# Performance work log

Hardware: AMD Instinct MI355X
Metric: run time of the kernel (lower is better)

Reference implementation:

```python
import jax, jax.numpy as jnp
import numpy as np

M_DIM = 1024
N_HEADS = 16
H_DIM = M_DIM // N_HEADS
FFN_H = 2 * M_DIM
B, S = 2, 2048
EPS = 1e-5
NEG = -1e9


def layernorm(x, g, b):
    mu = jnp.mean(x, axis=-1, keepdims=True)
    var = jnp.mean((x - mu) ** 2, axis=-1, keepdims=True)
    return (x - mu) * jax.lax.rsqrt(var + EPS) * g + b


def setup_inputs() -> dict:
    key = jax.random.key(0)
    ks = jax.random.split(key, 16)
    sc = 0.02
    return {
        "x": jax.random.normal(ks[0], (B, S, M_DIM), jnp.float32),
        "attention_mask": jnp.ones((B, S), jnp.int32),
        # per-head QKV projections stacked over heads: [H, M, D]
        "Wq": jax.random.normal(ks[1], (N_HEADS, M_DIM, H_DIM), jnp.float32) * sc,
        "bq": jnp.zeros((N_HEADS, H_DIM), jnp.float32),
        "Wk": jax.random.normal(ks[2], (N_HEADS, M_DIM, H_DIM), jnp.float32) * sc,
        "bk": jnp.zeros((N_HEADS, H_DIM), jnp.float32),
        "Wv": jax.random.normal(ks[3], (N_HEADS, M_DIM, H_DIM), jnp.float32) * sc,
        "bv": jnp.zeros((N_HEADS, H_DIM), jnp.float32),
        "Wo": jax.random.normal(ks[4], (M_DIM, M_DIM), jnp.float32) * sc,
        "bo": jnp.zeros((M_DIM,), jnp.float32),
        "g1": jnp.ones((M_DIM,), jnp.float32),
        "b1": jnp.zeros((M_DIM,), jnp.float32),
        "W1": jax.random.normal(ks[5], (M_DIM, FFN_H), jnp.float32) * sc,
        "bias1": jnp.zeros((FFN_H,), jnp.float32),
        "W2": jax.random.normal(ks[6], (FFN_H, M_DIM), jnp.float32) * sc,
        "bias2": jnp.zeros((M_DIM,), jnp.float32),
        "g2": jnp.ones((M_DIM,), jnp.float32),
        "b2": jnp.zeros((M_DIM,), jnp.float32),
    }


def reference(x, attention_mask, Wq, bq, Wk, bk, Wv, bv, Wo, bo, g1, b1, W1, bias1, W2, bias2, g2, b2):
    # All heads at once (the torch code loops over heads; same math).
    q = jnp.einsum("bsm,hmd->bhsd", x, Wq) + bq[None, :, None, :]
    k = jnp.einsum("bsm,hmd->bhsd", x, Wk) + bk[None, :, None, :]
    v = jnp.einsum("bsm,hmd->bhsd", x, Wv) + bv[None, :, None, :]
    scores = jnp.einsum("bhqd,bhkd->bhqk", q, k) / jnp.sqrt(jnp.float32(H_DIM))
    mask = attention_mask[:, None, None, :].astype(bool)  # [B,1,1,S] over keys
    scores = jnp.where(mask, scores, NEG)
    attn = jax.nn.softmax(scores, axis=-1)
    ctx = jnp.einsum("bhqk,bhkd->bhqd", attn, v)
    ctx = ctx.transpose(0, 2, 1, 3).reshape(x.shape[0], x.shape[1], M_DIM)  # concat heads
    out = ctx @ Wo + bo
    out = layernorm(out + x, g1, b1)
    fout = jax.nn.relu(out @ W1 + bias1) @ W2 + bias2
    out = layernorm(out + fout, g2, b2)
    return out
```

## Files before the change

kernel.cpp:

```cpp
#include <hip/hip_runtime.h>

#define MDIM 1024
#define FFH  2048
#define SEQ  2048
#define NEGV -1e9f
#define AST  72
#define QSCL 0.18033688f

#if __has_builtin(__builtin_amdgcn_exp2f)
  #define EXP2(x) __builtin_amdgcn_exp2f(x)
#else
  #define EXP2(x) exp2f(x)
#endif

typedef __attribute__((ext_vector_type(8))) __bf16 bf16x8;
typedef __attribute__((ext_vector_type(4))) float floatx4;
typedef __attribute__((address_space(3))) unsigned int lds_uint;
typedef const __attribute__((address_space(1))) unsigned int g_uint;

__device__ __forceinline__ unsigned short f2bf(float f){
  union { float f; unsigned u; } v; v.f = f;
  unsigned u = v.u;
  u += 0x7fffu + ((u >> 16) & 1u);
  return (unsigned short)(u >> 16);
}
__device__ __forceinline__ unsigned short f2bf_tr(float f){
  union { float f; unsigned u; } v; v.f = f;
  return (unsigned short)(v.u >> 16);
}

__global__ void k_cvt_bf16(const float* __restrict__ src, unsigned short* __restrict__ dst){
  int i = (blockIdx.x * 256 + threadIdx.x) * 4;
  float4 v = *(const float4*)(src + i);
  ushort4 o;
  o.x = f2bf(v.x); o.y = f2bf(v.y); o.z = f2bf(v.z); o.w = f2bf(v.w);
  *(ushort4*)(dst + i) = o;
}

__global__ void k_build_qbias(const float* __restrict__ bq, const float* __restrict__ bk,
                              const float* __restrict__ bv, float* __restrict__ dst){
  int i = blockIdx.x * 256 + threadIdx.x;
  dst[i] = (i < 1024) ? bq[i] * QSCL : (i < 2048) ? bk[i - 1024] : bv[i - 2048];
}

__global__ void __launch_bounds__(256) k_transpose_t(const float* __restrict__ src,
                                                     unsigned short* __restrict__ dst,
                                                     int K, int N){
  __shared__ unsigned short Ts[32 * 36];
  const int t = threadIdx.x;
  const int k0 = blockIdx.y << 5, n0 = blockIdx.x << 5;
  const int lr = t >> 3, lc4 = (t & 7) << 2;
  float4 v = *(const float4*)(src + (size_t)(k0 + lr) * N + n0 + lc4);
  ushort4 o; o.x = f2bf(v.x); o.y = f2bf(v.y); o.z = f2bf(v.z); o.w = f2bf(v.w);
  *(ushort4*)&Ts[lr * 36 + lc4] = o;
  __syncthreads();
  ushort4 w;
  w.x = Ts[(lc4 + 0) * 36 + lr];
  w.y = Ts[(lc4 + 1) * 36 + lr];
  w.z = Ts[(lc4 + 2) * 36 + lr];
  w.w = Ts[(lc4 + 3) * 36 + lr];
  *(ushort4*)(dst + (size_t)(n0 + lr) * K + k0 + lc4) = w;
}

__global__ void __launch_bounds__(256) k_build_wqkvt_t(const float* __restrict__ Wq,
                                                       const float* __restrict__ Wk,
                                                       const float* __restrict__ Wv,
                                                       unsigned short* __restrict__ dst){
  __shared__ unsigned short Ts[32 * 36];
  const int t = threadIdx.x;
  const int z = blockIdx.z;
  const int tensor = z >> 4, h = z & 15;
  const float* W = (tensor == 0) ? Wq : (tensor == 1) ? Wk : Wv;
  const float scl = (tensor == 0) ? QSCL : 1.0f;
  const int m0 = blockIdx.x << 5;
  const int d0 = blockIdx.y << 5;
  const int lr = t >> 3, lc4 = (t & 7) << 2;
  float4 v = *(const float4*)(W + ((size_t)h << 16) + (size_t)(m0 + lr) * 64 + d0 + lc4);
  ushort4 o; o.x = f2bf(v.x * scl); o.y = f2bf(v.y * scl); o.z = f2bf(v.z * scl); o.w = f2bf(v.w * scl);
  *(ushort4*)&Ts[lr * 36 + lc4] = o;
  __syncthreads();
  ushort4 w;
  w.x = Ts[(lc4 + 0) * 36 + lr];
  w.y = Ts[(lc4 + 1) * 36 + lr];
  w.z = Ts[(lc4 + 2) * 36 + lr];
  w.w = Ts[(lc4 + 3) * 36 + lr];
  const int n = (tensor << 10) + (h << 6) + d0 + lr;
  *(ushort4*)(dst + ((size_t)n << 10) + m0 + lc4) = w;
}

template<int RELU, int OUTBF>
__global__ void __launch_bounds__(256) k_gemm128(const unsigned short* __restrict__ A,
                                                 const unsigned short* __restrict__ Bt,
                                                 const float* __restrict__ bias,
                                                 void* __restrict__ Cout, int N, int K){
  __shared__ unsigned short As[2 * 128 * 32];
  __shared__ unsigned short Bs[2 * 128 * 32];
  const int t = threadIdx.x;
  const int m0 = blockIdx.y << 7, n0 = blockIdx.x << 7;
  const int lane = t & 63, w = t >> 6;
  const int quad = lane >> 4, l16 = lane & 15;
  const int mw = (w & 1) << 6, nw = (w >> 1) << 6;
  floatx4 acc[4][4];
  #pragma unroll
  for (int i = 0; i < 4; i++)
    #pragma unroll
    for (int j = 0; j < 4; j++) acc[i][j] = (floatx4){0.f, 0.f, 0.f, 0.f};
  const unsigned short* Ag  = A  + (size_t)(m0 + (t >> 2)) * K + ((t & 3) << 3);
  const unsigned short* Ag2 = Ag + (size_t)64 * K;
  const unsigned short* Bg  = Bt + (size_t)(n0 + (t >> 2)) * K + ((t & 3) << 3);
  const unsigned short* Bg2 = Bg + (size_t)64 * K;
  for (int kb = 0; kb < K; kb += 64){
    #pragma unroll
    for (int s = 0; s < 2; s++){
      const int ko = kb + (s << 5), lo = (s << 12) + (t << 3);
      __builtin_amdgcn_global_load_lds((g_uint*)(Ag  + ko), (lds_uint*)&As[lo],        16, 0, 0);
      __builtin_amdgcn_global_load_lds((g_uint*)(Ag2 + ko), (lds_uint*)&As[lo + 2048], 16, 0, 0);
      __builtin_amdgcn_global_load_lds((g_uint*)(Bg  + ko), (lds_uint*)&Bs[lo],        16, 0, 0);
      __builtin_amdgcn_global_load_lds((g_uint*)(Bg2 + ko), (lds_uint*)&Bs[lo + 2048], 16, 0, 0);
    }
    __syncthreads();
    #pragma unroll
    for (int s = 0; s < 2; s++){
      const int sb = s << 12;
      bf16x8 af[4], bf[4];
      #pragma unroll
      for (int mt = 0; mt < 4; mt++)
        af[mt] = *(const bf16x8*)&As[sb + ((mw + (mt << 4) + l16) << 5) + (quad << 3)];
      #pragma unroll
      for (int nt = 0; nt < 4; nt++)
        bf[nt] = *(const bf16x8*)&Bs[sb + ((nw + (nt << 4) + l16) << 5) + (quad << 3)];
      #pragma unroll
      for (int mt = 0; mt < 4; mt++)
        #pragma unroll
        for (int nt = 0; nt < 4; nt++)
          acc[mt][nt] = __builtin_amdgcn_mfma_f32_16x16x32_bf16(af[mt], bf[nt], acc[mt][nt], 0, 0, 0);
    }
    __syncthreads();
  }
  #pragma unroll
  for (int nt = 0; nt < 4; nt++){
    const int col = n0 + nw + (nt << 4) + l16;
    const float bsv = bias[col];
    #pragma unroll
    for (int mt = 0; mt < 4; mt++){
      const int row = m0 + mw + (mt << 4) + (quad << 2);
      #pragma unroll
      for (int r = 0; r < 4; r++){
        float v = acc[mt][nt][r] + bsv;
        if (RELU) v = fmaxf(v, 0.f);
        if (OUTBF) ((unsigned short*)Cout)[(size_t)(row + r) * N + col] = f2bf(v);
        else       ((float*)Cout)[(size_t)(row + r) * N + col] = v;
      }
    }
  }
}

template<int RELU, int OUTBF>
__global__ void __launch_bounds__(256) k_gemm64n(const unsigned short* __restrict__ A,
                                                 const unsigned short* __restrict__ Bt,
                                                 const float* __restrict__ bias,
                                                 void* __restrict__ Cout, int N, int K){
  __shared__ unsigned short As[2 * 128 * 32];
  __shared__ unsigned short Bs[2 * 64 * 32];
  const int t = threadIdx.x;
  const int m0 = blockIdx.y << 7, n0 = blockIdx.x << 6;
  const int lane = t & 63, w = t >> 6;
  const int quad = lane >> 4, l16 = lane & 15;
  const int mw = (w & 1) << 6, nw = (w >> 1) << 5;
  floatx4 acc[4][2];
  #pragma unroll
  for (int i = 0; i < 4; i++)
    #pragma unroll
    for (int j = 0; j < 2; j++) acc[i][j] = (floatx4){0.f, 0.f, 0.f, 0.f};
  const unsigned short* Ag  = A  + (size_t)(m0 + (t >> 2)) * K + ((t & 3) << 3);
  const unsigned short* Ag2 = Ag + (size_t)64 * K;
  const unsigned short* Bg  = Bt + (size_t)(n0 + (t >> 2)) * K + ((t & 3) << 3);
  for (int kb = 0; kb < K; kb += 64){
    #pragma unroll
    for (int s = 0; s < 2; s++){
      const int ko = kb + (s << 5);
      __builtin_amdgcn_global_load_lds((g_uint*)(Ag  + ko), (lds_uint*)&As[(s << 12) + (t << 3)],        16, 0, 0);
      __builtin_amdgcn_global_load_lds((g_uint*)(Ag2 + ko), (lds_uint*)&As[(s << 12) + (t << 3) + 2048], 16, 0, 0);
      __builtin_amdgcn_global_load_lds((g_uint*)(Bg  + ko), (lds_uint*)&Bs[(s << 11) + (t << 3)],        16, 0, 0);
    }
    __syncthreads();
    #pragma unroll
    for (int s = 0; s < 2; s++){
      bf16x8 af[4], bf[2];
      #pragma unroll
      for (int mt = 0; mt < 4; mt++)
        af[mt] = *(const bf16x8*)&As[(s << 12) + ((mw + (mt << 4) + l16) << 5) + (quad << 3)];
      #pragma unroll
      for (int nt = 0; nt < 2; nt++)
        bf[nt] = *(const bf16x8*)&Bs[(s << 11) + ((nw + (nt << 4) + l16) << 5) + (quad << 3)];
      #pragma unroll
      for (int mt = 0; mt < 4; mt++)
        #pragma unroll
        for (int nt = 0; nt < 2; nt++)
          acc[mt][nt] = __builtin_amdgcn_mfma_f32_16x16x32_bf16(af[mt], bf[nt], acc[mt][nt], 0, 0, 0);
    }
    __syncthreads();
  }
  #pragma unroll
  for (int nt = 0; nt < 2; nt++){
    const int col = n0 + nw + (nt << 4) + l16;
    const float bsv = bias[col];
    #pragma unroll
    for (int mt = 0; mt < 4; mt++){
      const int row = m0 + mw + (mt << 4) + (quad << 2);
      #pragma unroll
      for (int r = 0; r < 4; r++){
        float v = acc[mt][nt][r] + bsv;
        if (RELU) v = fmaxf(v, 0.f);
        if (OUTBF) ((unsigned short*)Cout)[(size_t)(row + r) * N + col] = f2bf(v);
        else       ((float*)Cout)[(size_t)(row + r) * N + col] = v;
      }
    }
  }
}

__global__ void __launch_bounds__(512) k_attn(const unsigned short* __restrict__ qkvb,
                                              const int* __restrict__ amask,
                                              unsigned short* __restrict__ ctxb){
  __shared__ __align__(16) unsigned short Ks[64 * AST];
  __shared__ __align__(16) unsigned short Vt[64 * AST];
  __shared__ __align__(16) unsigned short PQs[128 * AST];
  __shared__ int msk[64];
  const int t = threadIdx.x;
  const int w = t >> 6, lane = t & 63;
  const int quad = lane >> 4, l16 = lane & 15;
  const int b = blockIdx.y >> 4, h = blockIdx.y & 15;
  const int q0 = blockIdx.x << 7;
  const int myrow = (w << 4) + l16;
  const int sr = t >> 2, sc = (t & 3) << 4;
  const int kg = (t & 255) >> 4, dc = (t & 15) << 2;
  const int kr = (t & 255) >> 2, kc = (t & 3) << 4;

  {
    const unsigned short* qs = qkvb + (size_t)((b << 11) + q0 + sr) * 3072 + (h << 6) + sc;
    *(uint4*)&PQs[sr * AST + sc]     = *(const uint4*)qs;
    *(uint4*)&PQs[sr * AST + sc + 8] = *(const uint4*)(qs + 8);
  }
  __syncthreads();
  const bf16x8 qf0 = *(const bf16x8*)&PQs[myrow * AST + (quad << 3)];
  const bf16x8 qf1 = *(const bf16x8*)&PQs[myrow * AST + (quad << 3) + 32];

  floatx4 accO[4];
  #pragma unroll
  for (int i = 0; i < 4; i++) accO[i] = (floatx4){0.f, 0.f, 0.f, 0.f};
  float l_run = 0.f;

  const unsigned short* kbase = qkvb + (size_t)((b << 11) + kr) * 3072 + 1024 + (h << 6) + kc;
  const unsigned short* vbase = qkvb + (size_t)((b << 11) + (kg << 2)) * 3072 + 2048 + (h << 6) + dc;
  const int* mbase = amask + (b << 11);

  uint4 krA, krB;
  ushort4 vr0, vr1, vr2, vr3;
  int mreg = 1;
  if (t < 256){
    const unsigned short* vs = vbase;
    vr0 = *(const ushort4*)(vs);
    vr1 = *(const ushort4*)(vs + 3072);
    vr2 = *(const ushort4*)(vs + 2 * 3072);
    vr3 = *(const ushort4*)(vs + 3 * 3072);
    if (t < 64) mreg = mbase[t];
  } else {
    const unsigned short* ks = kbase;
    krA = *(const uint4*)ks;
    krB = *(const uint4*)(ks + 8);
  }

  for (int k0 = 0; k0 < SEQ; k0 += 64){
    __syncthreads();
    if (t < 256){
      ushort4 c;
      c.x = vr0.x; c.y = vr1.x; c.z = vr2.x; c.w = vr3.x; *(ushort4*)&Vt[(dc + 0) * AST + (kg << 2)] = c;
      c.x = vr0.y; c.y = vr1.y; c.z = vr2.y; c.w = vr3.y; *(ushort4*)&Vt[(dc + 1) * AST + (kg << 2)] = c;
      c.x = vr0.z; c.y = vr1.z; c.z = vr2.z; c.w = vr3.z; *(ushort4*)&Vt[(dc + 2) * AST + (kg << 2)] = c;
      c.x = vr0.w; c.y = vr1.w; c.z = vr2.w; c.w = vr3.w; *(ushort4*)&Vt[(dc + 3) * AST + (kg << 2)] = c;
      if (t < 64) msk[t] = mreg;
    } else {
      *(uint4*)&Ks[kr * AST + kc]     = krA;
      *(uint4*)&Ks[kr * AST + kc + 8] = krB;
    }
    __syncthreads();
    if (k0 + 64 < SEQ){
      if (t < 256){
        const unsigned short* vs = vbase + (size_t)(k0 + 64) * 3072;
        vr0 = *(const ushort4*)(vs);
        vr1 = *(const ushort4*)(vs + 3072);
        vr2 = *(const ushort4*)(vs + 2 * 3072);
        vr3 = *(const ushort4*)(vs + 3 * 3072);
        if (t < 64) mreg = mbase[k0 + 64 + t];
      } else {
        const unsigned short* ks = kbase + (size_t)(k0 + 64) * 3072;
        krA = *(const uint4*)ks;
        krB = *(const uint4*)(ks + 8);
      }
    }

    floatx4 st4[4];
    #pragma unroll
    for (int mt = 0; mt < 4; mt++){
      st4[mt] = (floatx4){0.f, 0.f, 0.f, 0.f};
      const unsigned short* kp = &Ks[((mt << 4) + l16) * AST + (quad << 3)];
      bf16x8 kf0 = *(const bf16x8*)(kp);
      bf16x8 kf1 = *(const bf16x8*)(kp + 32);
      st4[mt] = __builtin_amdgcn_mfma_f32_16x16x32_bf16(kf0, qf0, st4[mt], 0, 0, 0);
      st4[mt] = __builtin_amdgcn_mfma_f32_16x16x32_bf16(kf1, qf1, st4[mt], 0, 0, 0);
    }
    float pv[16], lsum = 0.f;
    #pragma unroll
    for (int mt = 0; mt < 4; mt++){
      const int4 m4 = *(const int4*)&msk[(mt << 4) + (quad << 2)];
      pv[mt * 4 + 0] = m4.x ? EXP2(st4[mt][0]) : 0.f;
      pv[mt * 4 + 1] = m4.y ? EXP2(st4[mt][1]) : 0.f;
      pv[mt * 4 + 2] = m4.z ? EXP2(st4[mt][2]) : 0.f;
      pv[mt * 4 + 3] = m4.w ? EXP2(st4[mt][3]) : 0.f;
    }
    #pragma unroll
    for (int e = 0; e < 16; e++) lsum += pv[e];
    lsum += __shfl_xor(lsum, 16);
    lsum += __shfl_xor(lsum, 32);
    l_run += lsum;
    #pragma unroll
    for (int mt = 0; mt < 4; mt++){
      ushort4 o;
      o.x = f2bf_tr(pv[mt * 4 + 0]);
      o.y = f2bf_tr(pv[mt * 4 + 1]);
      o.z = f2bf_tr(pv[mt * 4 + 2]);
      o.w = f2bf_tr(pv[mt * 4 + 3]);
      *(ushort4*)&PQs[myrow * AST + (mt << 4) + (quad << 2)] = o;
    }
    asm volatile("" ::: "memory");
    const bf16x8 pf0 = *(const bf16x8*)&PQs[myrow * AST + (quad << 3)];
    const bf16x8 pf1 = *(const bf16x8*)&PQs[myrow * AST + (quad << 3) + 32];
    #pragma unroll
    for (int mt = 0; mt < 4; mt++){
      const unsigned short* vp = &Vt[((mt << 4) + l16) * AST + (quad << 3)];
      bf16x8 vf0 = *(const bf16x8*)(vp);
      bf16x8 vf1 = *(const bf16x8*)(vp + 32);
      accO[mt] = __builtin_amdgcn_mfma_f32_16x16x32_bf16(vf0, pf0, accO[mt], 0, 0, 0);
      accO[mt] = __builtin_amdgcn_mfma_f32_16x16x32_bf16(vf1, pf1, accO[mt], 0, 0, 0);
    }
  }
  const float linv = 1.f / l_run;
  unsigned short* orow = ctxb + (size_t)((b << 11) + q0 + myrow) * 1024 + (h << 6);
  #pragma unroll
  for (int mt = 0; mt < 4; mt++){
    ushort4 o;
    o.x = f2bf(accO[mt][0] * linv);
    o.y = f2bf(accO[mt][1] * linv);
    o.z = f2bf(accO[mt][2] * linv);
    o.w = f2bf(accO[mt][3] * linv);
    *(ushort4*)&orow[(mt << 4) + (quad << 2)] = o;
  }
}

__global__ void __launch_bounds__(256) k_ln(const unsigned short* __restrict__ a,
                                            const float* __restrict__ res,
                                            const float* __restrict__ gg, const float* __restrict__ bb,
                                            float* __restrict__ out, unsigned short* __restrict__ outb){
  const int row = blockIdx.x, t = threadIdx.x;
  const ushort4 au = ((const ushort4*)(a + (size_t)row * 1024))[t];
  const float4 rv = ((const float4*)(res + (size_t)row * 1024))[t];
  float4 v;
  { union { unsigned u; float f; } c;
    c.u = (unsigned)au.x << 16; v.x = c.f + rv.x;
    c.u = (unsigned)au.y << 16; v.y = c.f + rv.y;
    c.u = (unsigned)au.z << 16; v.z = c.f + rv.z;
    c.u = (unsigned)au.w << 16; v.w = c.f + rv.w; }
  float sum = v.x + v.y + v.z + v.w;
  float ss  = v.x * v.x + v.y * v.y + v.z * v.z + v.w * v.w;
  #pragma unroll
  for (int off = 32; off > 0; off >>= 1){
    sum += __shfl_down(sum, off);
    ss  += __shfl_down(ss, off);
  }
  __shared__ float red[8];
  const int w = t >> 6;
  if ((t & 63) == 0){ red[w] = sum; red[4 + w] = ss; }
  __syncthreads();
  const float S  = red[0] + red[1] + red[2] + red[3];
  const float SS = red[4] + red[5] + red[6] + red[7];
  const float mu  = S * (1.f / 1024.f);
  const float var = SS * (1.f / 1024.f) - mu * mu;
  const float rs  = rsqrtf(var + 1e-5f);
  const float4 gv = ((const float4*)gg)[t];
  const float4 bv = ((const float4*)bb)[t];
  float4 o;
  o.x = (v.x - mu) * rs * gv.x + bv.x;
  o.y = (v.y - mu) * rs * gv.y + bv.y;
  o.z = (v.z - mu) * rs * gv.z + bv.z;
  o.w = (v.w - mu) * rs * gv.w + bv.w;
  ((float4*)(out + (size_t)row * 1024))[t] = o;
  if (outb){
    ushort4 ob; ob.x = f2bf(o.x); ob.y = f2bf(o.y); ob.z = f2bf(o.z); ob.w = f2bf(o.w);
    ((ushort4*)(outb + (size_t)row * 1024))[t] = ob;
  }
}

extern "C" void kernel_launch(void* const* d_in, const int* in_sizes, int n_in,
                              void* d_out, int out_size, void* d_ws, size_t ws_size,
                              hipStream_t stream){
  const float* x     = (const float*)d_in[0];
  const int*   amask = (const int*)d_in[1];
  const float* Wq    = (const float*)d_in[2];
  const float* bq    = (const float*)d_in[3];
  const float* Wk    = (const float*)d_in[4];
  const float* bk    = (const float*)d_in[5];
  const float* Wv    = (const float*)d_in[6];
  const float* bv    = (const float*)d_in[7];
  const float* Wo    = (const float*)d_in[8];
  const float* bo    = (const float*)d_in[9];
  const float* g1    = (const float*)d_in[10];
  const float* b1    = (const float*)d_in[11];
  const float* W1    = (const float*)d_in[12];
  const float* bias1 = (const float*)d_in[13];
  const float* W2    = (const float*)d_in[14];
  const float* bias2 = (const float*)d_in[15];
  const float* g2    = (const float*)d_in[16];
  const float* b2    = (const float*)d_in[17];

  char* ws = (char*)d_ws;
  unsigned short* xb    = (unsigned short*)(ws + 0);
  unsigned short* wqkvt = (unsigned short*)(ws + 8388608);
  float*          qbias = (float*)         (ws + 14680064);
  unsigned short* wot   = (unsigned short*)(ws + 14692352);
  unsigned short* w1t   = (unsigned short*)(ws + 16789504);
  unsigned short* w2t   = (unsigned short*)(ws + 20983808);
  unsigned short* ctxb  = (unsigned short*)(ws + 25178112);
  unsigned short* attnb = (unsigned short*)(ws + 33566720);
  unsigned short* fbufb = attnb;
  unsigned short* qkvb  = (unsigned short*)(ws + 50343936);
  float*          out1  = (float*)         (ws + 50343936);
  unsigned short* out1b = (unsigned short*)(ws + 50343936 + 25165824);
  unsigned short* h1    = (unsigned short*)(ws + 50343936 + 33554432);

  k_cvt_bf16      <<<dim3(4096),       dim3(256), 0, stream>>>(x, xb);
  k_build_wqkvt_t <<<dim3(32, 2, 48),  dim3(256), 0, stream>>>(Wq, Wk, Wv, wqkvt);
  k_build_qbias   <<<dim3(12),         dim3(256), 0, stream>>>(bq, bk, bv, qbias);
  k_transpose_t   <<<dim3(32, 32),     dim3(256), 0, stream>>>(Wo, wot, MDIM, MDIM);
  k_transpose_t   <<<dim3(64, 32),     dim3(256), 0, stream>>>(W1, w1t, MDIM, FFH);
  k_transpose_t   <<<dim3(32, 64),     dim3(256), 0, stream>>>(W2, w2t, FFH, MDIM);

  k_gemm128<0,1><<<dim3(24, 32), dim3(256), 0, stream>>>(xb, wqkvt, qbias, qkvb, 3072, 1024);
  k_attn<<<dim3(16, 32), dim3(512), 0, stream>>>(qkvb, amask, ctxb);
  k_gemm64n<0,1><<<dim3(16, 32), dim3(256), 0, stream>>>(ctxb, wot, bo, attnb, MDIM, 1024);
  k_ln<<<dim3(4096), dim3(256), 0, stream>>>(attnb, x, g1, b1, out1, out1b);
  k_gemm128<1,1><<<dim3(16, 32), dim3(256), 0, stream>>>(out1b, w1t, bias1, h1, FFH, 1024);
  k_gemm64n<0,1><<<dim3(16, 32), dim3(256), 0, stream>>>(h1, w2t, bias2, fbufb, MDIM, 2048);
  k_ln<<<dim3(4096), dim3(256), 0, stream>>>(fbufb, out1, g2, b2, (float*)d_out, nullptr);
}
```

Measured before the change: 341.1 us.

## Widen attention key tile to 128 and merge weight-prep kernels

The attention kernel now processes 128 keys per iteration instead of 64. All 512 threads load K and V rather than splitting them into producer halves, and launch bounds are set to request 4 waves per SIMD. This halves the number of barriers per sequence and gives more MFMA work between syncs, at the cost of more LDS and registers. Separately, six small prep launches are merged into two fused kernels to cut launch overhead.

```diff
diff --git a/kernel.cpp b/kernel.cpp
--- a/kernel.cpp
+++ b/kernel.cpp
@@ -3,8 +3,8 @@
 #define MDIM 1024
 #define FFH  2048
 #define SEQ  2048
-#define NEGV -1e9f
 #define AST  72
+#define VST  136
 #define QSCL 0.18033688f
 
 #if __has_builtin(__builtin_amdgcn_exp2f)
@@ -29,27 +29,63 @@
   return (unsigned short)(v.u >> 16);
 }
 
-__global__ void k_cvt_bf16(const float* __restrict__ src, unsigned short* __restrict__ dst){
-  int i = (blockIdx.x * 256 + threadIdx.x) * 4;
-  float4 v = *(const float4*)(src + i);
-  ushort4 o;
-  o.x = f2bf(v.x); o.y = f2bf(v.y); o.z = f2bf(v.z); o.w = f2bf(v.w);
-  *(ushort4*)(dst + i) = o;
-}
-
-__global__ void k_build_qbias(const float* __restrict__ bq, const float* __restrict__ bk,
-                              const float* __restrict__ bv, float* __restrict__ dst){
-  int i = blockIdx.x * 256 + threadIdx.x;
-  dst[i] = (i < 1024) ? bq[i] * QSCL : (i < 2048) ? bk[i - 1024] : bv[i - 2048];
-}
-
-__global__ void __launch_bounds__(256) k_transpose_t(const float* __restrict__ src,
-                                                     unsigned short* __restrict__ dst,
-                                                     int K, int N){
+__global__ void k_cvt_qb(const float* __restrict__ x, unsigned short* __restrict__ xb,
+                         const float* __restrict__ bq, const float* __restrict__ bk,
+                         const float* __restrict__ bv, float* __restrict__ qbias){
+  const int bid = blockIdx.x, t = threadIdx.x;
+  if (bid < 4096){
+    int i = (bid * 256 + t) * 4;
+    float4 v = *(const float4*)(x + i);
+    ushort4 o;
+    o.x = f2bf(v.x); o.y = f2bf(v.y); o.z = f2bf(v.z); o.w = f2bf(v.w);
+    *(ushort4*)(xb + i) = o;
+  } else {
+    int i = (bid - 4096) * 256 + t;
+    qbias[i] = (i < 1024) ? bq[i] * QSCL : (i < 2048) ? bk[i - 1024] : bv[i - 2048];
+  }
+}
+
+__global__ void __launch_bounds__(256) k_prep_w(const float* __restrict__ Wo, const float* __restrict__ W1,
+                                                const float* __restrict__ W2, const float* __restrict__ Wq,
+                                                const float* __restrict__ Wk, const float* __restrict__ Wv,
+                                                unsigned short* __restrict__ wot, unsigned short* __restrict__ w1t,
+                                                unsigned short* __restrict__ w2t, unsigned short* __restrict__ wqkvt){
   __shared__ unsigned short Ts[32 * 36];
-  const int t = threadIdx.x;
-  const int k0 = blockIdx.y << 5, n0 = blockIdx.x << 5;
+  const int t = threadIdx.x, bid = blockIdx.x;
   const int lr = t >> 3, lc4 = (t & 7) << 2;
+  if (bid >= 5120){
+    const int id = bid - 5120;
+    const int xm = id & 31, yd = (id >> 5) & 1, z = id >> 6;
+    const int tensor = z >> 4, h = z & 15;
+    const float* W = (tensor == 0) ? Wq : (tensor == 1) ? Wk : Wv;
+    const float scl = (tensor == 0) ? QSCL : 1.0f;
+    const int m0 = xm << 5, d0 = yd << 5;
+    float4 v = *(const float4*)(W + ((size_t)h << 16) + (size_t)(m0 + lr) * 64 + d0 + lc4);
+    ushort4 o; o.x = f2bf(v.x * scl); o.y = f2bf(v.y * scl); o.z = f2bf(v.z * scl); o.w = f2bf(v.w * scl);
+    *(ushort4*)&Ts[lr * 36 + lc4] = o;
+    __syncthreads();
+    ushort4 w;
+    w.x = Ts[(lc4 + 0) * 36 + lr];
+    w.y = Ts[(lc4 + 1) * 36 + lr];
+    w.z = Ts[(lc4 + 2) * 36 + lr];
+    w.w = Ts[(lc4 + 3) * 36 + lr];
+    const int n = (tensor << 10) + (h << 6) + d0 + lr;
+    *(ushort4*)(wqkvt + ((size_t)n << 10) + m0 + lc4) = w;
+    return;
+  }
+  const float* src; unsigned short* dst; int K, N, k0, n0;
+  if (bid < 1024){
+    src = Wo; dst = wot; K = 1024; N = 1024;
+    n0 = (bid & 31) << 5; k0 = (bid >> 5) << 5;
+  } else if (bid < 3072){
+    const int id = bid - 1024;
+    src = W1; dst = w1t; K = 1024; N = 2048;
+    n0 = (id & 63) << 5; k0 = (id >> 6) << 5;
+  } else {
+    const int id = bid - 3072;
+    src = W2; dst = w2t; K = 2048; N = 1024;
+    n0 = (id & 31) << 5; k0 = (id >> 5) << 5;
+  }
   float4 v = *(const float4*)(src + (size_t)(k0 + lr) * N + n0 + lc4);
   ushort4 o; o.x = f2bf(v.x); o.y = f2bf(v.y); o.z = f2bf(v.z); o.w = f2bf(v.w);
   *(ushort4*)&Ts[lr * 36 + lc4] = o;
@@ -60,32 +96,6 @@
   w.z = Ts[(lc4 + 2) * 36 + lr];
   w.w = Ts[(lc4 + 3) * 36 + lr];
   *(ushort4*)(dst + (size_t)(n0 + lr) * K + k0 + lc4) = w;
-}
-
-__global__ void __launch_bounds__(256) k_build_wqkvt_t(const float* __restrict__ Wq,
-                                                       const float* __restrict__ Wk,
-                                                       const float* __restrict__ Wv,
-                                                       unsigned short* __restrict__ dst){
-  __shared__ unsigned short Ts[32 * 36];
-  const int t = threadIdx.x;
-  const int z = blockIdx.z;
-  const int tensor = z >> 4, h = z & 15;
-  const float* W = (tensor == 0) ? Wq : (tensor == 1) ? Wk : Wv;
-  const float scl = (tensor == 0) ? QSCL : 1.0f;
-  const int m0 = blockIdx.x << 5;
-  const int d0 = blockIdx.y << 5;
-  const int lr = t >> 3, lc4 = (t & 7) << 2;
-  float4 v = *(const float4*)(W + ((size_t)h << 16) + (size_t)(m0 + lr) * 64 + d0 + lc4);
-  ushort4 o; o.x = f2bf(v.x * scl); o.y = f2bf(v.y * scl); o.z = f2bf(v.z * scl); o.w = f2bf(v.w * scl);
-  *(ushort4*)&Ts[lr * 36 + lc4] = o;
-  __syncthreads();
-  ushort4 w;
-  w.x = Ts[(lc4 + 0) * 36 + lr];
-  w.y = Ts[(lc4 + 1) * 36 + lr];
-  w.z = Ts[(lc4 + 2) * 36 + lr];
-  w.w = Ts[(lc4 + 3) * 36 + lr];
-  const int n = (tensor << 10) + (h << 6) + d0 + lr;
-  *(ushort4*)(dst + ((size_t)n << 10) + m0 + lc4) = w;
 }
 
 template<int RELU, int OUTBF>
@@ -219,13 +229,13 @@
   }
 }
 
-__global__ void __launch_bounds__(512) k_attn(const unsigned short* __restrict__ qkvb,
-                                              const int* __restrict__ amask,
-                                              unsigned short* __restrict__ ctxb){
-  __shared__ __align__(16) unsigned short Ks[64 * AST];
-  __shared__ __align__(16) unsigned short Vt[64 * AST];
-  __shared__ __align__(16) unsigned short PQs[128 * AST];
-  __shared__ int msk[64];
+__global__ void __launch_bounds__(512, 4) k_attn(const unsigned short* __restrict__ qkvb,
+                                                 const int* __restrict__ amask,
+                                                 unsigned short* __restrict__ ctxb){
+  __shared__ __align__(16) unsigned short Ks[128 * AST];
+  __shared__ __align__(16) unsigned short Vt[64 * VST];
+  __shared__ __align__(16) unsigned short PQs[128 * VST];
+  __shared__ int msk[128];
   const int t = threadIdx.x;
   const int w = t >> 6, lane = t & 63;
   const int quad = lane >> 4, l16 = lane & 15;
@@ -233,115 +243,101 @@
   const int q0 = blockIdx.x << 7;
   const int myrow = (w << 4) + l16;
   const int sr = t >> 2, sc = (t & 3) << 4;
-  const int kg = (t & 255) >> 4, dc = (t & 15) << 2;
-  const int kr = (t & 255) >> 2, kc = (t & 3) << 4;
+  const int kg = t >> 4, dc = (t & 15) << 2;
 
   {
     const unsigned short* qs = qkvb + (size_t)((b << 11) + q0 + sr) * 3072 + (h << 6) + sc;
-    *(uint4*)&PQs[sr * AST + sc]     = *(const uint4*)qs;
-    *(uint4*)&PQs[sr * AST + sc + 8] = *(const uint4*)(qs + 8);
+    *(uint4*)&PQs[sr * VST + sc]     = *(const uint4*)qs;
+    *(uint4*)&PQs[sr * VST + sc + 8] = *(const uint4*)(qs + 8);
   }
   __syncthreads();
-  const bf16x8 qf0 = *(const bf16x8*)&PQs[myrow * AST + (quad << 3)];
-  const bf16x8 qf1 = *(const bf16x8*)&PQs[myrow * AST + (quad << 3) + 32];
+  const bf16x8 qf0 = *(const bf16x8*)&PQs[myrow * VST + (quad << 3)];
+  const bf16x8 qf1 = *(const bf16x8*)&PQs[myrow * VST + (quad << 3) + 32];
 
   floatx4 accO[4];
   #pragma unroll
   for (int i = 0; i < 4; i++) accO[i] = (floatx4){0.f, 0.f, 0.f, 0.f};
   float l_run = 0.f;
 
-  const unsigned short* kbase = qkvb + (size_t)((b << 11) + kr) * 3072 + 1024 + (h << 6) + kc;
+  const unsigned short* kbase = qkvb + (size_t)((b << 11) + sr) * 3072 + 1024 + (h << 6) + sc;
   const unsigned short* vbase = qkvb + (size_t)((b << 11) + (kg << 2)) * 3072 + 2048 + (h << 6) + dc;
   const int* mbase = amask + (b << 11);
 
   uint4 krA, krB;
   ushort4 vr0, vr1, vr2, vr3;
   int mreg = 1;
-  if (t < 256){
+  {
+    const unsigned short* ks = kbase;
+    krA = *(const uint4*)ks;
+    krB = *(const uint4*)(ks + 8);
     const unsigned short* vs = vbase;
     vr0 = *(const ushort4*)(vs);
     vr1 = *(const ushort4*)(vs + 3072);
     vr2 = *(const ushort4*)(vs + 2 * 3072);
     vr3 = *(const ushort4*)(vs + 3 * 3072);
-    if (t < 64) mreg = mbase[t];
-  } else {
-    const unsigned short* ks = kbase;
-    krA = *(const uint4*)ks;
-    krB = *(const uint4*)(ks + 8);
-  }
-
-  for (int k0 = 0; k0 < SEQ; k0 += 64){
-    __syncthreads();
-    if (t < 256){
+    if (t < 128) mreg = mbase[t];
+  }
+
+  for (int k0 = 0; k0 < SEQ; k0 += 128){
+    __syncthreads();
+    *(uint4*)&Ks[sr * AST + sc]     = krA;
+    *(uint4*)&Ks[sr * AST + sc + 8] = krB;
+    {
       ushort4 c;
-      c.x = vr0.x; c.y = vr1.x; c.z = vr2.x; c.w = vr3.x; *(ushort4*)&Vt[(dc + 0) * AST + (kg << 2)] = c;
-      c.x = vr0.y; c.y = vr1.y; c.z = vr2.y; c.w = vr3.y; *(ushort4*)&Vt[(dc + 1) * AST + (kg << 2)] = c;
-      c.x = vr0.z; c.y = vr1.z; c.z = vr2.z; c.w = vr3.z; *(ushort4*)&Vt[(dc + 2) * AST + (kg << 2)] = c;
-      c.x = vr0.w; c.y = vr1.w; c.z = vr2.w; c.w = vr3.w; *(ushort4*)&Vt[(dc + 3) * AST + (kg << 2)] = c;
-      if (t < 64) msk[t] = mreg;
-    } else {
-      *(uint4*)&Ks[kr * AST + kc]     = krA;
-      *(uint4*)&Ks[kr * AST + kc + 8] = krB;
-    }
-    __syncthreads();
-    if (k0 + 64 < SEQ){
-      if (t < 256){
-        const unsigned short* vs = vbase + (size_t)(k0 + 64) * 3072;
-        vr0 = *(const ushort4*)(vs);
-        vr1 = *(const ushort4*)(vs + 3072);
-        vr2 = *(const ushort4*)(vs + 2 * 3072);
-        vr3 = *(const ushort4*)(vs + 3 * 3072);
-        if (t < 64) mreg = mbase[k0 + 64 + t];
-      } else {
-        const unsigned short* ks = kbase + (size_t)(k0 + 64) * 3072;
-        krA = *(const uint4*)ks;
-        krB = *(const uint4*)(ks + 8);
-      }
-    }
-
-    floatx4 st4[4];
-    #pragma unroll
-    for (int mt = 0; mt < 4; mt++){
-      st4[mt] = (floatx4){0.f, 0.f, 0.f, 0.f};
+      c.x = vr0.x; c.y = vr1.x; c.z = vr2.x; c.w = vr3.x; *(ushort4*)&Vt[(dc + 0) * VST + (kg << 2)] = c;
+      c.x = vr0.y; c.y = vr1.y; c.z = vr2.y; c.w = vr3.y; *(ushort4*)&Vt[(dc + 1) * VST + (kg << 2)] = c;
+      c.x = vr0.z; c.y = vr1.z; c.z = vr2.z; c.w = vr3.z; *(ushort4*)&Vt[(dc + 2) * VST + (kg << 2)] = c;
+      c.x = vr0.w; c.y = vr1.w; c.z = vr2.w; c.w = vr3.w; *(ushort4*)&Vt[(dc + 3) * VST + (kg << 2)] = c;
+    }
+    if (t < 128) msk[t] = mreg;
+    __syncthreads();
+    if (k0 + 128 < SEQ){
+      const unsigned short* ks = kbase + (size_t)(k0 + 128) * 3072;
+      krA = *(const uint4*)ks;
+      krB = *(const uint4*)(ks + 8);
+      const unsigned short* vs = vbase + (size_t)(k0 + 128) * 3072;
+      vr0 = *(const ushort4*)(vs);
+      vr1 = *(const ushort4*)(vs + 3072);
+      vr2 = *(const ushort4*)(vs + 2 * 3072);
+      vr3 = *(const ushort4*)(vs + 3 * 3072);
+      if (t < 128) mreg = mbase[k0 + 128 + t];
+    }
+
+    float lsum = 0.f;
+    #pragma unroll
+    for (int mt = 0; mt < 8; mt++){
+      floatx4 st = (floatx4){0.f, 0.f, 0.f, 0.f};
       const unsigned short* kp = &Ks[((mt << 4) + l16) * AST + (quad << 3)];
       bf16x8 kf0 = *(const bf16x8*)(kp);
       bf16x8 kf1 = *(const bf16x8*)(kp + 32);
-      st4[mt] = __builtin_amdgcn_mfma_f32_16x16x32_bf16(kf0, qf0, st4[mt], 0, 0, 0);
-      st4[mt] = __builtin_amdgcn_mfma_f32_16x16x32_bf16(kf1, qf1, st4[mt], 0, 0, 0);
-    }
-    float pv[16], lsum = 0.f;
-    #pragma unroll
-    for (int mt = 0; mt < 4; mt++){
+      st = __builtin_amdgcn_mfma_f32_16x16x32_bf16(kf0, qf0, st, 0, 0, 0);
+      st = __builtin_amdgcn_mfma_f32_16x16x32_bf16(kf1, qf1, st, 0, 0, 0);
       const int4 m4 = *(const int4*)&msk[(mt << 4) + (quad << 2)];
-      pv[mt * 4 + 0] = m4.x ? EXP2(st4[mt][0]) : 0.f;
-      pv[mt * 4 + 1] = m4.y ? EXP2(st4[mt][1]) : 0.f;
-      pv[mt * 4 + 2] = m4.z ? EXP2(st4[mt][2]) : 0.f;
-      pv[mt * 4 + 3] = m4.w ? EXP2(st4[mt][3]) : 0.f;
-    }
-    #pragma unroll
-    for (int e = 0; e < 16; e++) lsum += pv[e];
+      float p0 = m4.x ? EXP2(st[0]) : 0.f;
+      float p1 = m4.y ? EXP2(st[1]) : 0.f;
+      float p2 = m4.z ? EXP2(st[2]) : 0.f;
+      float p3 = m4.w ? EXP2(st[3]) : 0.f;
+      lsum += p0 + p1 + p2 + p3;
+      ushort4 o;
+      o.x = f2bf_tr(p0); o.y = f2bf_tr(p1); o.z = f2bf_tr(p2); o.w = f2bf_tr(p3);
+      *(ushort4*)&PQs[myrow * VST + (mt << 4) + (quad << 2)] = o;
+    }
     lsum += __shfl_xor(lsum, 16);
     lsum += __shfl_xor(lsum, 32);
     l_run += lsum;
+    asm volatile("" ::: "memory");
+    bf16x8 pf[4];
+    #pragma unroll
+    for (int s = 0; s < 4; s++)
+      pf[s] = *(const bf16x8*)&PQs[myrow * VST + (s << 5) + (quad << 3)];
     #pragma unroll
     for (int mt = 0; mt < 4; mt++){
-      ushort4 o;
-      o.x = f2bf_tr(pv[mt * 4 + 0]);
-      o.y = f2bf_tr(pv[mt * 4 + 1]);
-      o.z = f2bf_tr(pv[mt * 4 + 2]);
-      o.w = f2bf_tr(pv[mt * 4 + 3]);
-      *(ushort4*)&PQs[myrow * AST + (mt << 4) + (quad << 2)] = o;
-    }
-    asm volatile("" ::: "memory");
-    const bf16x8 pf0 = *(const bf16x8*)&PQs[myrow * AST + (quad << 3)];
-    const bf16x8 pf1 = *(const bf16x8*)&PQs[myrow * AST + (quad << 3) + 32];
-    #pragma unroll
-    for (int mt = 0; mt < 4; mt++){
-      const unsigned short* vp = &Vt[((mt << 4) + l16) * AST + (quad << 3)];
-      bf16x8 vf0 = *(const bf16x8*)(vp);
-      bf16x8 vf1 = *(const bf16x8*)(vp + 32);
-      accO[mt] = __builtin_amdgcn_mfma_f32_16x16x32_bf16(vf0, pf0, accO[mt], 0, 0, 0);
-      accO[mt] = __builtin_amdgcn_mfma_f32_16x16x32_bf16(vf1, pf1, accO[mt], 0, 0, 0);
+      const unsigned short* vp = &Vt[((mt << 4) + l16) * VST + (quad << 3)];
+      #pragma unroll
+      for (int s = 0; s < 4; s++){
+        bf16x8 vf = *(const bf16x8*)(vp + (s << 5));
+        accO[mt] = __builtin_amdgcn_mfma_f32_16x16x32_bf16(vf, pf[s], accO[mt], 0, 0, 0);
+      }
     }
   }
   const float linv = 1.f / l_run;
@@ -437,12 +433,8 @@
   unsigned short* out1b = (unsigned short*)(ws + 50343936 + 25165824);
   unsigned short* h1    = (unsigned short*)(ws + 50343936 + 33554432);
 
-  k_cvt_bf16      <<<dim3(4096),       dim3(256), 0, stream>>>(x, xb);
-  k_build_wqkvt_t <<<dim3(32, 2, 48),  dim3(256), 0, stream>>>(Wq, Wk, Wv, wqkvt);
-  k_build_qbias   <<<dim3(12),         dim3(256), 0, stream>>>(bq, bk, bv, qbias);
-  k_transpose_t   <<<dim3(32, 32),     dim3(256), 0, stream>>>(Wo, wot, MDIM, MDIM);
-  k_transpose_t   <<<dim3(64, 32),     dim3(256), 0, stream>>>(W1, w1t, MDIM, FFH);
-  k_transpose_t   <<<dim3(32, 64),     dim3(256), 0, stream>>>(W2, w2t, FFH, MDIM);
+  k_cvt_qb<<<dim3(4108), dim3(256), 0, stream>>>(x, xb, bq, bk, bv, qbias);
+  k_prep_w<<<dim3(8192), dim3(256), 0, stream>>>(Wo, W1, W2, Wq, Wk, Wv, wot, w1t, w2t, wqkvt);
 
   k_gemm128<0,1><<<dim3(24, 32), dim3(256), 0, stream>>>(xb, wqkvt, qbias, qkvb, 3072, 1024);
   k_attn<<<dim3(16, 32), dim3(512), 0, stream>>>(qkvb, amask, ctxb);
```

Measured after the change: 336.2 us. Within noise of the previous version (-1.4%).
